# Optimization experiments

Hardware: AMD Instinct MI355X
Metric: run time of the kernel (lower is better)

The kernel has to match this reference:

```python
import jax, jax.numpy as jnp
import numpy as np

N, LQ, DM = 8, 2500, 256
NH, NL, NP, NZ = 8, 4, 8, 4
DH = DM // NH
SPATIAL = np.array([[64, 176], [32, 88], [16, 44], [8, 22]], dtype=np.int32)
LEN_IN = int((SPATIAL[:, 0] * SPATIAL[:, 1]).sum())


def setup_inputs() -> dict:
    key = jax.random.key(0)
    ks = jax.random.split(key, 10)
    query = jax.random.normal(ks[0], (N, LQ, DM), dtype=jnp.float32)
    query_pos = jax.random.normal(ks[1], (N, LQ, DM), dtype=jnp.float32)
    reference_points = jax.random.uniform(ks[2], (N, LQ, NZ, 2), dtype=jnp.float32)
    input_flatten = jax.random.normal(ks[3], (N, LEN_IN, DM), dtype=jnp.float32)
    input_spatial_shapes = jnp.asarray(SPATIAL)
    lsi = np.concatenate([[0], np.cumsum(SPATIAL[:, 0] * SPATIAL[:, 1])[:-1]]).astype(np.int32)
    input_level_start_index = jnp.asarray(lsi)
    # learned params (Linear: y = x @ W + b, W is (in, out))
    Wv = jax.random.normal(ks[4], (DM, DM), dtype=jnp.float32) * (1.0 / np.sqrt(DM))
    bv = jnp.zeros((DM,), dtype=jnp.float32)
    Wo = jax.random.normal(ks[5], (DM, NH * NL * NP * 2), dtype=jnp.float32) * 0.02
    bo = jax.random.normal(ks[6], (NH * NL * NP * 2,), dtype=jnp.float32) * 1.0
    Wa = jax.random.normal(ks[7], (DM, NH * NL * NP), dtype=jnp.float32) * 0.02
    ba = jnp.zeros((NH * NL * NP,), dtype=jnp.float32)
    return {"query": query, "query_pos": query_pos, "reference_points": reference_points,
            "input_flatten": input_flatten, "input_spatial_shapes": input_spatial_shapes,
            "input_level_start_index": input_level_start_index,
            "Wv": Wv, "bv": bv, "Wo": Wo, "bo": bo, "Wa": Wa, "ba": ba}


def _sample_level(v, h, w, loc):
    """Bilinear sample (grid_sample, align_corners=False, zero padding).
    v:   (N, h*w, NH, DH) level feature map
    loc: (N, Lq, NH, P, 2) normalized locations in [0,1] (x, y)
    returns (N, NH, Lq, P, DH)
    """
    n, hw, nh, dh = v.shape
    lq, p = loc.shape[1], loc.shape[3]
    x = loc[..., 0] * w - 0.5
    y = loc[..., 1] * h - 0.5
    x0f = jnp.floor(x)
    y0f = jnp.floor(y)
    wx = x - x0f
    wy = y - y0f
    x0 = x0f.astype(jnp.int32)
    y0 = y0f.astype(jnp.int32)
    vt = v.transpose(0, 2, 1, 3).reshape(n * nh, hw, dh)

    def gather(xi, yi, wgt):
        valid = ((xi >= 0) & (xi < w) & (yi >= 0) & (yi < h)).astype(v.dtype)
        idx = jnp.clip(yi, 0, h - 1) * w + jnp.clip(xi, 0, w - 1)  # (N,Lq,NH,P)
        idx = idx.transpose(0, 2, 1, 3).reshape(n * nh, lq * p)
        g = jnp.take_along_axis(vt, idx[:, :, None], axis=1)  # (N*NH, Lq*P, DH)
        wv = (wgt * valid).transpose(0, 2, 1, 3).reshape(n * nh, lq * p)
        return g * wv[:, :, None]

    out = (gather(x0, y0, (1 - wx) * (1 - wy))
           + gather(x0 + 1, y0, wx * (1 - wy))
           + gather(x0, y0 + 1, (1 - wx) * wy)
           + gather(x0 + 1, y0 + 1, wx * wy))
    return out.reshape(n, nh, lq, p, dh)


def _forward(query, query_pos, reference_points, input_flatten, spatial, Wv, bv, Wo, bo, Wa, ba):
    n, lq, _ = query.shape
    len_in = input_flatten.shape[1]
    # projections
    value = (input_flatten @ Wv + bv).reshape(n, len_in, NH, DH)
    off = (query @ Wo + bo).reshape(n, lq, NH, NL, NP, 2)
    aw = jax.nn.softmax((query @ Wa + ba).reshape(n, lq, NH, NL * NP), axis=-1)
    aw = aw.reshape(n, lq, NH, NL, NP)
    # normalize offsets by (W_l, H_l), add to Z-anchor reference points
    norm = jnp.asarray(np.stack([spatial[:, 1], spatial[:, 0]], -1), dtype=query.dtype)  # (NL,2)
    off = off / norm[None, None, None, :, None, :]
    off = off.reshape(n, lq, NH, NL, NP // NZ, NZ, 2)
    ref = reference_points[:, :, None, None, None, :, :]  # (N,Lq,1,1,1,NZ,2)
    loc = (ref + off).reshape(n, lq, NH, NL, NP, 2)
    # multi-scale deformable sampling + weighted reduction
    out = jnp.zeros((n, lq, NH, DH), dtype=query.dtype)
    start = 0
    for lvl in range(NL):
        h, w = int(spatial[lvl, 0]), int(spatial[lvl, 1])
        v_l = value[:, start:start + h * w]
        start += h * w
        samp = _sample_level(v_l, h, w, loc[:, :, :, lvl])  # (N,NH,Lq,NP,DH)
        out = out + jnp.einsum('nhqpd,nqhp->nqhd', samp, aw[:, :, :, lvl])
    return out.reshape(n, lq, DM)


def reference(query, query_pos, reference_points, input_flatten, input_spatial_shapes,
              input_level_start_index, Wv, bv, Wo, bo, Wa, ba):
    spatial = np.asarray(jax.device_get(input_spatial_shapes))
    return _forward(query, query_pos, reference_points, input_flatten, spatial,
                    Wv, bv, Wo, bo, Wa, ba)
```

## Files before the change

kernel.cpp:

```cpp
#include <hip/hip_runtime.h>
#include <hip/hip_fp16.h>

#define N_BATCH 8
#define LQ_     2500
#define DM_     256
#define NH_     8
#define NL_     4
#define NP_     8
#define DH_     32
#define LEN_IN_ 14960
#define KDIM    256

#define MV_   119680
#define MQ_   20000
#define NBMQ  157

__constant__ int c_w[4]     = {176, 88, 44, 22};
__constant__ int c_h[4]     = {64, 32, 16, 8};
__constant__ int c_start[4] = {0, 11264, 14080, 14784};

using bf16x8 = __attribute__((ext_vector_type(8))) short;
using f32x4  = __attribute__((ext_vector_type(4))) float;

#define GLDS16(g, l)                                                         \
    __builtin_amdgcn_global_load_lds(                                        \
        (const __attribute__((address_space(1))) void*)(g),                  \
        (__attribute__((address_space(3))) void*)(l), 16, 0, 0)

static __device__ inline float fdot2_u(unsigned int p, unsigned int w, float c) {
    float r;
    asm("v_dot2_f32_f16 %0, %1, %2, %3" : "=v"(r) : "v"(p), "v"(w), "v"(c));
    return r;
}

static __device__ inline void split_bf16(float v, unsigned short& hi, unsigned short& lo) {
    unsigned int u = __float_as_uint(v);
    hi = (unsigned short)(u >> 16);
    float hif = __uint_as_float(u & 0xFFFF0000u);
    float l = v - hif;
    lo = (unsigned short)(__float_as_uint(l) >> 16);
}

static __device__ inline unsigned short f2bf_rne(float v) {
    unsigned int u = __float_as_uint(v);
    u += 0x7FFFu + ((u >> 16) & 1u);
    return (unsigned short)(u >> 16);
}

static __device__ inline unsigned short f2h_rne(float v) {
    _Float16 h = (_Float16)v;
    return __builtin_bit_cast(unsigned short, h);
}

static __device__ inline ushort4 cvt4_rne(float4 v) {
    ushort4 h;
    h.x = f2bf_rne(v.x);
    h.y = f2bf_rne(v.y);
    h.z = f2bf_rne(v.z);
    h.w = f2bf_rne(v.w);
    return h;
}

__global__ __launch_bounds__(256) void cast_bf16(
    const float* __restrict__ src, unsigned short* __restrict__ dst, int n8)
{
    const float4* s = (const float4*)src;
    ushort4*      d = (ushort4*)dst;
    int i = blockIdx.x * 256 + threadIdx.x;
    const int st = gridDim.x * 256;
    for (; i < n8; i += st) {
        float4 a = s[2 * i], b = s[2 * i + 1];
        d[2 * i]     = cvt4_rne(a);
        d[2 * i + 1] = cvt4_rne(b);
    }
}

__global__ __launch_bounds__(256) void conv_weights(
    const float* __restrict__ Wv, const float* __restrict__ Wo,
    const float* __restrict__ Wa, const float* __restrict__ bo,
    const float* __restrict__ ba,
    unsigned short* __restrict__ Wv_hi, unsigned short* __restrict__ Wv_lo,
    unsigned short* __restrict__ Wc_hi, unsigned short* __restrict__ Wc_lo,
    float* __restrict__ bcomb)
{
    int id = blockIdx.x * 256 + threadIdx.x;
    if (id < 256 * 256) {
        int n = id >> 8, k = id & 255;
        unsigned short h, l;
        split_bf16(Wv[k * 256 + n], h, l);
        Wv_hi[id] = h; Wv_lo[id] = l;
    } else {
        int id2 = id - 65536;
        if (id2 < 768 * 256) {
            int n = id2 >> 8, k = id2 & 255;
            float v = (n < 512) ? Wo[k * 512 + n] : Wa[k * 256 + (n - 512)];
            unsigned short h, l;
            split_bf16(v, h, l);
            Wc_hi[id2] = h; Wc_lo[id2] = l;
        }
    }
    if (id < 768) bcomb[id] = (id < 512) ? bo[id] : ba[id - 512];
}

template <bool F16_OUT, bool XSWIZ>
__global__ __launch_bounds__(512, 6) void gemm_glds(
    const unsigned short* __restrict__ Abf,
    const unsigned short* __restrict__ Bth,
    const unsigned short* __restrict__ Btl,
    const float* __restrict__ bias,
    float* __restrict__ C,
    unsigned short* __restrict__ Cb,
    int M, int N, int nbm)
{
    __shared__ __align__(16) unsigned short As [4096];
    __shared__ __align__(16) unsigned short Bhs[4096];
    __shared__ __align__(16) unsigned short Bls[4096];

    const int tid = threadIdx.x;
    const int ntn = N >> 7;
    int by, bx;
    if (XSWIZ) {
        int xcd = blockIdx.x & 7, j = blockIdx.x >> 3;
        by = xcd + 8 * (j / ntn);
        bx = j % ntn;
        if (by >= nbm) return;
    } else {
        by = blockIdx.x >> 1;
        bx = blockIdx.x & 1;
    }
    const int row0 = by << 7, col0 = bx << 7;
    const int lane = tid & 63, wave = tid >> 6;
    const int wrow = (wave & 1) << 6, wcol = (wave >> 1) << 5;
    const int r16  = lane & 15, quad = lane >> 4;

    const int srow = tid >> 2, skq = tid & 3;
    const int arow = min(row0 + srow, M - 1);
    const unsigned short* gA  = Abf + (size_t)arow * KDIM + skq * 8;
    const unsigned short* gBh = Bth + (size_t)(col0 + srow) * KDIM + skq * 8;
    const unsigned short* gBl = Btl + (size_t)(col0 + srow) * KDIM + skq * 8;
    unsigned short* lA  = &As [wave << 9];
    unsigned short* lBh = &Bhs[wave << 9];
    unsigned short* lBl = &Bls[wave << 9];

    f32x4 acc[4][2];
#pragma unroll
    for (int i = 0; i < 4; ++i)
#pragma unroll
        for (int j = 0; j < 2; ++j) acc[i][j] = (f32x4){0.f, 0.f, 0.f, 0.f};

#pragma unroll
    for (int kt = 0; kt < 8; ++kt) {
        GLDS16(gA  + kt * 32, lA);
        GLDS16(gBh + kt * 32, lBh);
        GLDS16(gBl + kt * 32, lBl);
        __syncthreads();

        bf16x8 fbh[2], fbl[2], fa[4];
#pragma unroll
        for (int tn = 0; tn < 2; ++tn) {
            int n = wcol + tn * 16 + r16;
            fbh[tn] = *(const bf16x8*)&Bhs[n * 32 + (quad << 3)];
            fbl[tn] = *(const bf16x8*)&Bls[n * 32 + (quad << 3)];
        }
#pragma unroll
        for (int tm = 0; tm < 4; ++tm)
            fa[tm] = *(const bf16x8*)&As[(wrow + tm * 16 + r16) * 32 + (quad << 3)];
#pragma unroll
        for (int tm = 0; tm < 4; ++tm)
#pragma unroll
            for (int tn = 0; tn < 2; ++tn) {
                acc[tm][tn] = __builtin_amdgcn_mfma_f32_16x16x32_bf16(fa[tm], fbl[tn], acc[tm][tn], 0, 0, 0);
                acc[tm][tn] = __builtin_amdgcn_mfma_f32_16x16x32_bf16(fa[tm], fbh[tn], acc[tm][tn], 0, 0, 0);
            }
        __syncthreads();
    }

    float bvs[2];
#pragma unroll
    for (int tn = 0; tn < 2; ++tn) bvs[tn] = bias[col0 + wcol + tn * 16 + r16];
#pragma unroll
    for (int tm = 0; tm < 4; ++tm) {
#pragma unroll
        for (int i = 0; i < 4; ++i) {
            int row = row0 + wrow + tm * 16 + (quad << 2) + i;
            if (row < M) {
                if (!F16_OUT) {
                    float* crow = C + (size_t)row * N + col0 + wcol + r16;
#pragma unroll
                    for (int tn = 0; tn < 2; ++tn)
                        crow[tn * 16] = acc[tm][tn][i] + bvs[tn];
                } else {
                    int n   = row / LEN_IN_;
                    int pix = row - n * LEN_IN_;
#pragma unroll
                    for (int tn = 0; tn < 2; ++tn) {
                        int col = col0 + wcol + tn * 16 + r16;
                        int h = col >> 5, dh = col & 31;
                        size_t addr = ((size_t)(n * NH_ + h) * LEN_IN_ + pix) * DH_ + dh;
                        Cb[addr] = f2h_rne(acc[tm][tn][i] + bvs[tn]);
                    }
                }
            }
        }
    }
}

__global__ __launch_bounds__(256, 4) void ms_sample(
    const unsigned short* __restrict__ value,
    const float* __restrict__ comb,
    const float* __restrict__ ref_pts,
    float* __restrict__ out)
{
    __shared__ uint4 s_desc[64][33];

    const int b     = blockIdx.x;
    const int xcd   = b & 7;
    const int j     = b >> 3;
    const int slice = (j / 40) * 8 + xcd;
    const int chunk = j % 40;
    const int n     = slice >> 3, h = slice & 7;
    const int q0    = chunk * 64;
    const int tid   = threadIdx.x;

    {
        int ql = tid >> 2, l = tid & 3;
        int q  = q0 + ql;
        if (q < LQ_) {
            int nq = n * LQ_ + q;
            const float* row = comb + (size_t)nq * 768;

            float4 L0 = *(const float4*)&row[512 + h * 32 + l * 8];
            float4 L1 = *(const float4*)&row[512 + h * 32 + l * 8 + 4];
            float lg[8] = {L0.x, L0.y, L0.z, L0.w, L1.x, L1.y, L1.z, L1.w};
            float m = lg[0];
#pragma unroll
            for (int i = 1; i < 8; ++i) m = fmaxf(m, lg[i]);
            m = fmaxf(m, __shfl_xor(m, 1));
            m = fmaxf(m, __shfl_xor(m, 2));
            float e[8], s = 0.f;
#pragma unroll
            for (int i = 0; i < 8; ++i) { e[i] = __expf(lg[i] - m); s += e[i]; }
            s += __shfl_xor(s, 1);
            s += __shfl_xor(s, 2);
            float inv = 1.f / s;

            float4 R0 = *(const float4*)&ref_pts[(size_t)nq * 8];
            float4 R1 = *(const float4*)&ref_pts[(size_t)nq * 8 + 4];
            float rx[4] = {R0.x, R0.z, R1.x, R1.z};
            float ry[4] = {R0.y, R0.w, R1.y, R1.w};

            float off[16];
#pragma unroll
            for (int i = 0; i < 4; ++i)
                *(float4*)&off[i * 4] = *(const float4*)&row[h * 64 + l * 16 + i * 4];

            float wl = (float)c_w[l], hl = (float)c_h[l];
            int wli = c_w[l], hli = c_h[l], st = c_start[l];
#pragma unroll
            for (int p = 0; p < 8; ++p) {
                int z = p & 3;
                float a = e[p] * inv;
                float x = rx[z] * wl + off[p * 2 + 0] - 0.5f;
                float y = ry[z] * hl + off[p * 2 + 1] - 0.5f;
                float x0f = floorf(x), y0f = floorf(y);
                int   x0 = (int)x0f,  y0 = (int)y0f;
                float wx = x - x0f,   wy = y - y0f;
                unsigned short ix[4];
                float wt[4];
#pragma unroll
                for (int jj = 0; jj < 4; ++jj) {
                    int xi = x0 + (jj & 1);
                    int yi = y0 + (jj >> 1);
                    float w = ((jj & 1) ? wx : 1.f - wx) * ((jj >> 1) ? wy : 1.f - wy);
                    bool valid = (xi >= 0) && (xi < wli) && (yi >= 0) && (yi < hli);
                    int xc = min(max(xi, 0), wli - 1);
                    int yc = min(max(yi, 0), hli - 1);
                    ix[jj] = (unsigned short)(yc * wli + xc);
                    wt[jj] = valid ? a * w : 0.f;
                }
                uint4 d;
                d.x = (unsigned int)(st + ix[0]) | ((unsigned int)(st + ix[1]) << 16);
                d.y = (unsigned int)(st + ix[2]) | ((unsigned int)(st + ix[3]) << 16);
                __half2 h01 = __floats2half2_rn(wt[0], wt[1]);
                __half2 h23 = __floats2half2_rn(wt[2], wt[3]);
                d.z = *(unsigned int*)&h01;
                d.w = *(unsigned int*)&h23;
                s_desc[ql][l * 8 + p] = d;
            }
        }
    }
    __syncthreads();

    int ql = tid >> 2, dhg = tid & 3;
    int q  = q0 + ql;
    if (q >= LQ_) return;
    int nq = n * LQ_ + q;
    const unsigned short* vb = value
        + ((size_t)(n * NH_ + h) * LEN_IN_) * DH_ + dhg * 8;

    float acc[8];
#pragma unroll
    for (int i = 0; i < 8; ++i) acc[i] = 0.f;

#pragma unroll 4
    for (int s = 0; s < 32; ++s) {
        uint4 d = s_desc[ql][s];
        int i0 = d.x & 0xFFFF, i1 = d.x >> 16;
        int i2 = d.y & 0xFFFF, i3 = d.y >> 16;
        uint4 v0 = *(const uint4*)(vb + i0 * DH_);
        uint4 v1 = *(const uint4*)(vb + i1 * DH_);
        uint4 v2 = *(const uint4*)(vb + i2 * DH_);
        uint4 v3 = *(const uint4*)(vb + i3 * DH_);
        acc[0] = fdot2_u(__builtin_amdgcn_perm(v1.x, v0.x, 0x05040100u), d.z, acc[0]);
        acc[1] = fdot2_u(__builtin_amdgcn_perm(v1.x, v0.x, 0x07060302u), d.z, acc[1]);
        acc[2] = fdot2_u(__builtin_amdgcn_perm(v1.y, v0.y, 0x05040100u), d.z, acc[2]);
        acc[3] = fdot2_u(__builtin_amdgcn_perm(v1.y, v0.y, 0x07060302u), d.z, acc[3]);
        acc[4] = fdot2_u(__builtin_amdgcn_perm(v1.z, v0.z, 0x05040100u), d.z, acc[4]);
        acc[5] = fdot2_u(__builtin_amdgcn_perm(v1.z, v0.z, 0x07060302u), d.z, acc[5]);
        acc[6] = fdot2_u(__builtin_amdgcn_perm(v1.w, v0.w, 0x05040100u), d.z, acc[6]);
        acc[7] = fdot2_u(__builtin_amdgcn_perm(v1.w, v0.w, 0x07060302u), d.z, acc[7]);
        acc[0] = fdot2_u(__builtin_amdgcn_perm(v3.x, v2.x, 0x05040100u), d.w, acc[0]);
        acc[1] = fdot2_u(__builtin_amdgcn_perm(v3.x, v2.x, 0x07060302u), d.w, acc[1]);
        acc[2] = fdot2_u(__builtin_amdgcn_perm(v3.y, v2.y, 0x05040100u), d.w, acc[2]);
        acc[3] = fdot2_u(__builtin_amdgcn_perm(v3.y, v2.y, 0x07060302u), d.w, acc[3]);
        acc[4] = fdot2_u(__builtin_amdgcn_perm(v3.z, v2.z, 0x05040100u), d.w, acc[4]);
        acc[5] = fdot2_u(__builtin_amdgcn_perm(v3.z, v2.z, 0x07060302u), d.w, acc[5]);
        acc[6] = fdot2_u(__builtin_amdgcn_perm(v3.w, v2.w, 0x05040100u), d.w, acc[6]);
        acc[7] = fdot2_u(__builtin_amdgcn_perm(v3.w, v2.w, 0x07060302u), d.w, acc[7]);
    }

    float* op = out + (size_t)nq * 256 + h * 32 + dhg * 8;
    *(float4*)&op[0] = make_float4(acc[0], acc[1], acc[2], acc[3]);
    *(float4*)&op[4] = make_float4(acc[4], acc[5], acc[6], acc[7]);
}

extern "C" void kernel_launch(void* const* d_in, const int* in_sizes, int n_in,
                              void* d_out, int out_size, void* d_ws, size_t ws_size,
                              hipStream_t stream)
{
    const float* query         = (const float*)d_in[0];
    const float* ref_pts       = (const float*)d_in[2];
    const float* input_flatten = (const float*)d_in[3];
    const float* Wv            = (const float*)d_in[6];
    const float* bv            = (const float*)d_in[7];
    const float* Wo            = (const float*)d_in[8];
    const float* bo            = (const float*)d_in[9];
    const float* Wa            = (const float*)d_in[10];
    const float* ba            = (const float*)d_in[11];
    float* out = (float*)d_out;

    char* ws = (char*)d_ws;
    size_t o = 0;
    unsigned short* Wv_hi = (unsigned short*)(ws + o); o += 256 * 256 * 2;
    unsigned short* Wv_lo = (unsigned short*)(ws + o); o += 256 * 256 * 2;
    unsigned short* Wc_hi = (unsigned short*)(ws + o); o += 768 * 256 * 2;
    unsigned short* Wc_lo = (unsigned short*)(ws + o); o += 768 * 256 * 2;
    float*          bcomb = (float*)(ws + o);          o += 768 * 4;
    o = (o + 511) & ~(size_t)511;
    unsigned short* value = (unsigned short*)(ws + o); o += (size_t)119680 * 256 * 2;
    o = (o + 511) & ~(size_t)511;
    float* combq = (float*)(ws + o); o += (size_t)20000 * 768 * 4;

    unsigned short* Abf_v = (unsigned short*)combq;
    unsigned short* Abf_q = (unsigned short*)d_out;

    hipLaunchKernelGGL(conv_weights, dim3(1024), dim3(256), 0, stream,
                       Wv, Wo, Wa, bo, ba, Wv_hi, Wv_lo, Wc_hi, Wc_lo, bcomb);
    hipLaunchKernelGGL(cast_bf16, dim3(2048), dim3(256), 0, stream,
                       input_flatten, Abf_v, MV_ * KDIM / 8);
    hipLaunchKernelGGL(cast_bf16, dim3(1024), dim3(256), 0, stream,
                       query, Abf_q, MQ_ * KDIM / 8);
    hipLaunchKernelGGL((gemm_glds<true, false>), dim3((MV_ / 128) * 2), dim3(512), 0, stream,
                       Abf_v, Wv_hi, Wv_lo, bv, (float*)nullptr, value, MV_, 256, 0);
    hipLaunchKernelGGL((gemm_glds<false, true>), dim3(8 * 20 * 6), dim3(512), 0, stream,
                       Abf_q, Wc_hi, Wc_lo, bcomb, combq, (unsigned short*)nullptr, MQ_, 768, NBMQ);
    hipLaunchKernelGGL(ms_sample, dim3(2560), dim3(256), 0, stream,
                       value, combq, ref_pts, out);
}
```

Baseline: 365.3 us.

## Merge prep kernels into one launch and both GEMMs into one grid

The weight conversion and the two bf16 casts become a single block-partitioned prep kernel. The value-projection and offset/attention GEMMs become a single launch whose blocks branch by block id, with XCD-swizzled tile mapping now also applied to the value GEMM. Occupancy launch bound rises from 6 to 8. The bf16 copy of input_flatten moves to its own workspace buffer so the GEMMs can run concurrently. This removes three kernel launches and the tail gaps between dependent kernels, at the cost of more workspace and possible register pressure from the runtime branch.

```diff
diff --git a/kernel.cpp b/kernel.cpp
--- a/kernel.cpp
+++ b/kernel.cpp
@@ -13,7 +13,10 @@
 
 #define MV_   119680
 #define MQ_   20000
+#define NBMV  935
 #define NBMQ  157
+#define NVB   1872
+#define NCB   960
 
 __constant__ int c_w[4]     = {176, 88, 44, 22};
 __constant__ int c_h[4]     = {64, 32, 16, 8};
@@ -61,73 +64,89 @@
     return h;
 }
 
-__global__ __launch_bounds__(256) void cast_bf16(
-    const float* __restrict__ src, unsigned short* __restrict__ dst, int n8)
-{
-    const float4* s = (const float4*)src;
-    ushort4*      d = (ushort4*)dst;
-    int i = blockIdx.x * 256 + threadIdx.x;
-    const int st = gridDim.x * 256;
-    for (; i < n8; i += st) {
-        float4 a = s[2 * i], b = s[2 * i + 1];
-        d[2 * i]     = cvt4_rne(a);
-        d[2 * i + 1] = cvt4_rne(b);
-    }
-}
-
-__global__ __launch_bounds__(256) void conv_weights(
+__global__ __launch_bounds__(256) void prep(
     const float* __restrict__ Wv, const float* __restrict__ Wo,
     const float* __restrict__ Wa, const float* __restrict__ bo,
     const float* __restrict__ ba,
+    const float* __restrict__ input_flatten, const float* __restrict__ query,
     unsigned short* __restrict__ Wv_hi, unsigned short* __restrict__ Wv_lo,
     unsigned short* __restrict__ Wc_hi, unsigned short* __restrict__ Wc_lo,
-    float* __restrict__ bcomb)
+    float* __restrict__ bcomb,
+    unsigned short* __restrict__ Abf_v, unsigned short* __restrict__ Abf_q)
 {
-    int id = blockIdx.x * 256 + threadIdx.x;
-    if (id < 256 * 256) {
-        int n = id >> 8, k = id & 255;
-        unsigned short h, l;
-        split_bf16(Wv[k * 256 + n], h, l);
-        Wv_hi[id] = h; Wv_lo[id] = l;
+    const int b = blockIdx.x, tid = threadIdx.x;
+    if (b < 2048) {
+        const float4* s = (const float4*)input_flatten;
+        ushort4*      d = (ushort4*)Abf_v;
+        const int n8 = MV_ * KDIM / 8, st = 2048 * 256;
+        for (int i = b * 256 + tid; i < n8; i += st) {
+            d[2 * i]     = cvt4_rne(s[2 * i]);
+            d[2 * i + 1] = cvt4_rne(s[2 * i + 1]);
+        }
+    } else if (b < 2560) {
+        const float4* s = (const float4*)query;
+        ushort4*      d = (ushort4*)Abf_q;
+        const int n8 = MQ_ * KDIM / 8, st = 512 * 256;
+        for (int i = (b - 2048) * 256 + tid; i < n8; i += st) {
+            d[2 * i]     = cvt4_rne(s[2 * i]);
+            d[2 * i + 1] = cvt4_rne(s[2 * i + 1]);
+        }
     } else {
-        int id2 = id - 65536;
-        if (id2 < 768 * 256) {
-            int n = id2 >> 8, k = id2 & 255;
-            float v = (n < 512) ? Wo[k * 512 + n] : Wa[k * 256 + (n - 512)];
-            unsigned short h, l;
-            split_bf16(v, h, l);
-            Wc_hi[id2] = h; Wc_lo[id2] = l;
-        }
-    }
-    if (id < 768) bcomb[id] = (id < 512) ? bo[id] : ba[id - 512];
-}
-
-template <bool F16_OUT, bool XSWIZ>
-__global__ __launch_bounds__(512, 6) void gemm_glds(
-    const unsigned short* __restrict__ Abf,
-    const unsigned short* __restrict__ Bth,
-    const unsigned short* __restrict__ Btl,
-    const float* __restrict__ bias,
-    float* __restrict__ C,
-    unsigned short* __restrict__ Cb,
-    int M, int N, int nbm)
+        const int base = (b - 2560) * 256 + tid;
+        for (int id = base; id < 262144; id += 131072) {
+            if (id < 65536) {
+                int n = id >> 8, k = id & 255;
+                unsigned short h, l;
+                split_bf16(Wv[k * 256 + n], h, l);
+                Wv_hi[id] = h; Wv_lo[id] = l;
+            } else {
+                int id2 = id - 65536;
+                int n = id2 >> 8, k = id2 & 255;
+                float v = (n < 512) ? Wo[k * 512 + n] : Wa[k * 256 + (n - 512)];
+                unsigned short h, l;
+                split_bf16(v, h, l);
+                Wc_hi[id2] = h; Wc_lo[id2] = l;
+            }
+        }
+        if (base < 768) bcomb[base] = (base < 512) ? bo[base] : ba[base - 512];
+    }
+}
+
+__global__ __launch_bounds__(512, 8) void gemm2(
+    const unsigned short* __restrict__ Av,
+    const unsigned short* __restrict__ Aq,
+    const unsigned short* __restrict__ Wvh, const unsigned short* __restrict__ Wvl,
+    const unsigned short* __restrict__ Wch, const unsigned short* __restrict__ Wcl,
+    const float* __restrict__ bv, const float* __restrict__ bc,
+    float* __restrict__ Cq,
+    unsigned short* __restrict__ Cv)
 {
     __shared__ __align__(16) unsigned short As [4096];
     __shared__ __align__(16) unsigned short Bhs[4096];
     __shared__ __align__(16) unsigned short Bls[4096];
 
     const int tid = threadIdx.x;
-    const int ntn = N >> 7;
-    int by, bx;
-    if (XSWIZ) {
-        int xcd = blockIdx.x & 7, j = blockIdx.x >> 3;
-        by = xcd + 8 * (j / ntn);
-        bx = j % ntn;
-        if (by >= nbm) return;
+    const int bid = blockIdx.x;
+    const bool is_comb = (bid >= NVB);
+
+    const unsigned short *A, *Bth, *Btl;
+    const float* bias;
+    int by, bx, M, N;
+    if (is_comb) {
+        int cid = bid - NVB;
+        int xcd = cid & 7, j = cid >> 3;
+        by = xcd + 8 * (j / 6); bx = j % 6;
+        if (by >= NBMQ) return;
+        A = Aq; Bth = Wch; Btl = Wcl; bias = bc;
+        M = MQ_; N = 768;
     } else {
-        by = blockIdx.x >> 1;
-        bx = blockIdx.x & 1;
-    }
+        int xcd = bid & 7, j = bid >> 3;
+        by = xcd + 8 * (j >> 1); bx = j & 1;
+        if (by >= NBMV) return;
+        A = Av; Bth = Wvh; Btl = Wvl; bias = bv;
+        M = MV_; N = 256;
+    }
+
     const int row0 = by << 7, col0 = bx << 7;
     const int lane = tid & 63, wave = tid >> 6;
     const int wrow = (wave & 1) << 6, wcol = (wave >> 1) << 5;
@@ -135,7 +154,7 @@
 
     const int srow = tid >> 2, skq = tid & 3;
     const int arow = min(row0 + srow, M - 1);
-    const unsigned short* gA  = Abf + (size_t)arow * KDIM + skq * 8;
+    const unsigned short* gA  = A   + (size_t)arow * KDIM + skq * 8;
     const unsigned short* gBh = Bth + (size_t)(col0 + srow) * KDIM + skq * 8;
     const unsigned short* gBl = Btl + (size_t)(col0 + srow) * KDIM + skq * 8;
     unsigned short* lA  = &As [wave << 9];
@@ -184,8 +203,8 @@
         for (int i = 0; i < 4; ++i) {
             int row = row0 + wrow + tm * 16 + (quad << 2) + i;
             if (row < M) {
-                if (!F16_OUT) {
-                    float* crow = C + (size_t)row * N + col0 + wcol + r16;
+                if (is_comb) {
+                    float* crow = Cq + (size_t)row * N + col0 + wcol + r16;
 #pragma unroll
                     for (int tn = 0; tn < 2; ++tn)
                         crow[tn * 16] = acc[tm][tn][i] + bvs[tn];
@@ -197,7 +216,7 @@
                         int col = col0 + wcol + tn * 16 + r16;
                         int h = col >> 5, dh = col & 31;
                         size_t addr = ((size_t)(n * NH_ + h) * LEN_IN_ + pix) * DH_ + dh;
-                        Cb[addr] = f2h_rne(acc[tm][tn][i] + bvs[tn]);
+                        Cv[addr] = f2h_rne(acc[tm][tn][i] + bvs[tn]);
                     }
                 }
             }
@@ -360,20 +379,16 @@
     unsigned short* value = (unsigned short*)(ws + o); o += (size_t)119680 * 256 * 2;
     o = (o + 511) & ~(size_t)511;
     float* combq = (float*)(ws + o); o += (size_t)20000 * 768 * 4;
-
-    unsigned short* Abf_v = (unsigned short*)combq;
+    o = (o + 511) & ~(size_t)511;
+    unsigned short* Abf_v = (unsigned short*)(ws + o); o += (size_t)MV_ * KDIM * 2;
     unsigned short* Abf_q = (unsigned short*)d_out;
 
-    hipLaunchKernelGGL(conv_weights, dim3(1024), dim3(256), 0, stream,
-                       Wv, Wo, Wa, bo, ba, Wv_hi, Wv_lo, Wc_hi, Wc_lo, bcomb);
-    hipLaunchKernelGGL(cast_bf16, dim3(2048), dim3(256), 0, stream,
-                       input_flatten, Abf_v, MV_ * KDIM / 8);
-    hipLaunchKernelGGL(cast_bf16, dim3(1024), dim3(256), 0, stream,
-                       query, Abf_q, MQ_ * KDIM / 8);
-    hipLaunchKernelGGL((gemm_glds<true, false>), dim3((MV_ / 128) * 2), dim3(512), 0, stream,
-                       Abf_v, Wv_hi, Wv_lo, bv, (float*)nullptr, value, MV_, 256, 0);
-    hipLaunchKernelGGL((gemm_glds<false, true>), dim3(8 * 20 * 6), dim3(512), 0, stream,
-                       Abf_q, Wc_hi, Wc_lo, bcomb, combq, (unsigned short*)nullptr, MQ_, 768, NBMQ);
+    hipLaunchKernelGGL(prep, dim3(3072), dim3(256), 0, stream,
+                       Wv, Wo, Wa, bo, ba, input_flatten, query,
+                       Wv_hi, Wv_lo, Wc_hi, Wc_lo, bcomb, Abf_v, Abf_q);
+    hipLaunchKernelGGL(gemm2, dim3(NVB + NCB), dim3(512), 0, stream,
+                       Abf_v, Abf_q, Wv_hi, Wv_lo, Wc_hi, Wc_lo,
+                       bv, bcomb, combq, value);
     hipLaunchKernelGGL(ms_sample, dim3(2560), dim3(256), 0, stream,
                        value, combq, ref_pts, out);
 }
```

Result: faster. 355.8 us (-2.6%).
